# Performance work log

Hardware: AMD Instinct MI355X
Metric: run time of the kernel (lower is better)

The kernel has to match this reference:

```python
import jax, jax.numpy as jnp
import numpy as np

B, D, N, K, H = 8, 1024, 4096, 64, 512


def setup_inputs() -> dict:
    key = jax.random.key(0)
    ks = jax.random.split(key, 8)
    s1 = 1.0 / np.sqrt(D)
    s2 = 1.0 / np.sqrt(H)
    return {
        "feature": jax.random.normal(ks[0], (B, D, N), jnp.float32),
        "xyz": jax.random.normal(ks[1], (B, 3, N), jnp.float32),
        "w1": jax.random.normal(ks[2], (H, D), jnp.float32) * s1,
        "b1": jnp.zeros((H,), jnp.float32),
        "g1": jnp.ones((H,), jnp.float32),
        "be1": jnp.zeros((H,), jnp.float32),
        "w2": jax.random.normal(ks[3], (H, H), jnp.float32) * s2,
        "b2": jnp.zeros((H,), jnp.float32),
        "g2": jnp.ones((H,), jnp.float32),
        "be2": jnp.zeros((H,), jnp.float32),
        "w3": jax.random.normal(ks[4], (K, H), jnp.float32) * s2,
        "b3": jnp.zeros((K,), jnp.float32),
    }


def _conv1d(x, w, b):
    # pointwise Conv1d (kernel_size=1): [b,c,n] x [o,c] -> [b,o,n]
    return jnp.einsum('bcn,oc->bon', x, w) + b[None, :, None]


def _bn(x, g, be, eps=1e-5):
    # BatchNorm1d in training mode: batch statistics over (batch, spatial)
    m = x.mean(axis=(0, 2), keepdims=True)
    v = x.var(axis=(0, 2), keepdims=True)
    return (x - m) * jax.lax.rsqrt(v + eps) * g[None, :, None] + be[None, :, None]


def _regular(center, reg=1e-4):
    k = center.shape[-1]
    gram = jnp.einsum('bdm,bdn->bmn', center, center)
    return reg * jnp.abs(gram - jnp.eye(k, dtype=center.dtype)[None]).mean()


def _sinkhorn(cost, epsilon, max_iter):
    # log-domain Sinkhorn with uniform marginals; fixed iteration count
    b, n, m = cost.shape
    log_p = jnp.full((b, n), -np.log(n), cost.dtype)
    log_q = jnp.full((b, m), -np.log(m), cost.dtype)

    def M(u, v):
        return (-cost + u[:, :, None] + v[:, None, :]) / epsilon

    def body(i, uv):
        u, v = uv
        u = epsilon * (log_p - jax.nn.logsumexp(M(u, v), axis=-1)) + u
        v = epsilon * (log_q - jax.nn.logsumexp(M(u, v), axis=-2)) + v
        return (u, v)

    u0 = jnp.zeros((b, n), cost.dtype)
    v0 = jnp.zeros((b, m), cost.dtype)
    u, v = jax.lax.fori_loop(0, max_iter, body, (u0, v0))
    return jnp.exp(M(u, v))  # transport plan gamma [b,n,m]


def _ot_assign(x, y, epsilon=1e-3, max_iter=25, dst='fe'):
    # x: [b,d,n], y: [b,d,m]
    if dst == 'eu':
        xn = jnp.sum(x * x, axis=1)  # [b,n]
        yn = jnp.sum(y * y, axis=1)  # [b,m]
        cost = xn[:, :, None] + yn[:, None, :] - 2.0 * jnp.einsum('bdn,bdm->bnm', x, y)
    else:
        cost = 2.0 - 2.0 * jnp.einsum('bdn,bdm->bnm', x, y)
    return _sinkhorn(cost, epsilon, max_iter)


def _normalize(x, axis=1, eps=1e-12):
    nrm = jnp.linalg.norm(x, axis=axis, keepdims=True)
    return x / jnp.maximum(nrm, eps)


def reference(feature, xyz, w1, b1, g1, be1, w2, b2, g2, be2, w3, b3):
    b, d, n = feature.shape
    h = jax.nn.relu(_bn(_conv1d(feature, w1, b1), g1, be1))
    h = jax.nn.relu(_bn(_conv1d(h, w2, b2), g2, be2))
    log_score = _conv1d(h, w3, b3)  # [b,K,n]
    score = jax.nn.softmax(log_score, axis=1)
    pi = jax.lax.stop_gradient(jnp.maximum(score.sum(-1), 1e-4))[:, None, :]  # [b,1,K]

    # xyz branch
    mu_xyz = jnp.einsum('bkn,bdn->bdk', score, xyz) / pi  # [b,3,K]
    reg_xyz = 0.001 * _regular(mu_xyz)
    gamma_xyz = _ot_assign(jax.lax.stop_gradient(xyz), jax.lax.stop_gradient(mu_xyz), dst='eu')
    assign_xyz = jax.lax.stop_gradient(n * jnp.swapaxes(gamma_xyz, -1, -2))  # [b,K,n]

    # feature branch
    mu_fea = jnp.einsum('bkn,bdn->bdk', score, feature) / pi  # [b,D,K]
    n_feature = _normalize(feature)
    n_mu = _normalize(mu_fea)
    reg_fea = _regular(n_mu)
    gamma_fea = _ot_assign(jax.lax.stop_gradient(n_feature), jax.lax.stop_gradient(n_mu), dst='fe')
    assign_fea = jax.lax.stop_gradient(n * jnp.swapaxes(gamma_fea, -1, -2))  # [b,K,n]

    logp = jax.nn.log_softmax(log_score, axis=1)
    loss_xyz = -jnp.mean(jnp.sum(assign_xyz * logp, axis=1))
    loss_fea = -jnp.mean(jnp.sum(assign_fea * logp, axis=1))
    return loss_xyz + loss_fea + reg_fea + reg_xyz
```

## Files before the change

### kernel.cpp

```cpp
#include <hip/hip_runtime.h>
#include <math.h>

#define B_ 8
#define D_ 1024
#define N_ 4096
#define K_ 64
#define H_ 512

typedef short sx8 __attribute__((ext_vector_type(8)));
typedef float fx4 __attribute__((ext_vector_type(4)));

__device__ __forceinline__ float block_reduce_sum256(float v, float* sm) {
  int tid = threadIdx.x;
  sm[tid] = v;
  __syncthreads();
  for (int s = 128; s > 0; s >>= 1) {
    if (tid < s) sm[tid] += sm[tid + s];
    __syncthreads();
  }
  float r = sm[0];
  __syncthreads();
  return r;
}

__device__ __forceinline__ ushort f2bf(float f) {
  unsigned u = __float_as_uint(f);
  unsigned r = (u + 0x7fffu + ((u >> 16) & 1u)) >> 16;
  return (ushort)r;
}
__device__ __forceinline__ float bf2f(ushort h) {
  return __uint_as_float(((unsigned)h) << 16);
}

__global__ __launch_bounds__(256)
void split_w3(const float* __restrict__ W1, const float* __restrict__ W2,
              const float* __restrict__ W3, ushort* __restrict__ Wh1,
              ushort* __restrict__ Wl1, ushort* __restrict__ Wh2,
              ushort* __restrict__ Wl2, ushort* __restrict__ Wh3,
              ushort* __restrict__ Wl3) {
  int i = blockIdx.x * 256 + threadIdx.x;
  const float* W;
  ushort *Wh, *Wl;
  int o;
  if (i < 524288) { W = W1; Wh = Wh1; Wl = Wl1; o = i; }
  else if (i < 786432) { W = W2; Wh = Wh2; Wl = Wl2; o = i - 524288; }
  else { W = W3; Wh = Wh3; Wl = Wl3; o = i - 786432; }
  float f = W[o];
  ushort h = f2bf(f);
  Wh[o] = h;
  Wl[o] = f2bf(f - bf2f(h));
}

__global__ __launch_bounds__(256)
void transpose_split(const float* __restrict__ F, ushort* __restrict__ FhT,
                     ushort* __restrict__ FlT, float* __restrict__ nrmsq) {
  __shared__ float tile[64][65];
  __shared__ float nsq[64];
  int b = blockIdx.z, d0 = blockIdx.y * 64, n0 = blockIdx.x * 64;
  const float* src = F + ((long)b * D_ + d0) * N_ + n0;
  int t = threadIdx.x;
  if (t < 64) nsq[t] = 0.f;
  int rr4 = t >> 4, c4 = (t & 15) * 4;
#pragma unroll
  for (int p = 0; p < 4; ++p) {
    int dr = p * 16 + rr4;
    float4 v = *(const float4*)(src + (long)dr * N_ + c4);
    tile[dr][c4 + 0] = v.x;
    tile[dr][c4 + 1] = v.y;
    tile[dr][c4 + 2] = v.z;
    tile[dr][c4 + 3] = v.w;
  }
  __syncthreads();
  int nlb = t >> 3, ds = (t & 7) * 8;
#pragma unroll
  for (int p = 0; p < 2; ++p) {
    int nl = p * 32 + nlb;
    sx8 hv, lv;
    float sq = 0.f;
#pragma unroll
    for (int j = 0; j < 8; ++j) {
      float f = tile[ds + j][nl];
      sq += f * f;
      ushort h = f2bf(f);
      hv[j] = (short)h;
      lv[j] = (short)f2bf(f - bf2f(h));
    }
    atomicAdd(&nsq[nl], sq);
    long o = ((long)b * N_ + n0 + nl) * D_ + d0 + ds;
    *(sx8*)(FhT + o) = hv;
    *(sx8*)(FlT + o) = lv;
  }
  __syncthreads();
  if (t < 64) atomicAdd(&nrmsq[(long)b * N_ + n0 + t], nsq[t]);
}

__global__ __launch_bounds__(256)
void gemm_split_bf16(const ushort* __restrict__ Ah, const ushort* __restrict__ Al,
                     const ushort* __restrict__ BhT, const ushort* __restrict__ BlT,
                     float* __restrict__ C, const float* __restrict__ bias,
                     int N, int Kd, long sBT, long sC) {
  __shared__ ushort As[2][128][40];
  __shared__ ushort Bs[2][128][40];
  const int t = threadIdx.x;
  const int m0 = blockIdx.y * 128, n0 = blockIdx.x * 128;
  const long bo = (long)blockIdx.z * sBT;
  float* Cp = C + (long)blockIdx.z * sC;
  const int half = t >> 7, r = t & 127;
  const ushort* Asrc = (half ? Al : Ah) + (long)(m0 + r) * Kd;
  const ushort* Bsrc = (half ? BlT : BhT) + bo + (long)(n0 + r) * Kd;
  ushort* AsD = &As[half][r][0];
  ushort* BsD = &Bs[half][r][0];
  const int w = t >> 6, ln = t & 15, qd = (t & 63) >> 4;
  const int wm = w >> 1, wn = w & 1;

  fx4 acc[4][4];
#pragma unroll
  for (int i = 0; i < 4; ++i)
#pragma unroll
    for (int j = 0; j < 4; ++j) acc[i][j] = (fx4)0.f;

  for (int k0 = 0; k0 < Kd; k0 += 32) {
    uint4 a0 = *(const uint4*)(Asrc + k0);
    uint4 a1 = *(const uint4*)(Asrc + k0 + 8);
    uint4 a2 = *(const uint4*)(Asrc + k0 + 16);
    uint4 a3 = *(const uint4*)(Asrc + k0 + 24);
    uint4 b0 = *(const uint4*)(Bsrc + k0);
    uint4 b1 = *(const uint4*)(Bsrc + k0 + 8);
    uint4 b2 = *(const uint4*)(Bsrc + k0 + 16);
    uint4 b3 = *(const uint4*)(Bsrc + k0 + 24);
    __syncthreads();
    *(uint4*)(AsD + 0) = a0;
    *(uint4*)(AsD + 8) = a1;
    *(uint4*)(AsD + 16) = a2;
    *(uint4*)(AsD + 24) = a3;
    *(uint4*)(BsD + 0) = b0;
    *(uint4*)(BsD + 8) = b1;
    *(uint4*)(BsD + 16) = b2;
    *(uint4*)(BsD + 24) = b3;
    __syncthreads();
    sx8 ahf[4], alf[4], bhf[4], blf[4];
#pragma unroll
    for (int mt = 0; mt < 4; ++mt) {
      ahf[mt] = *(const sx8*)&As[0][wm * 64 + mt * 16 + ln][qd * 8];
      alf[mt] = *(const sx8*)&As[1][wm * 64 + mt * 16 + ln][qd * 8];
    }
#pragma unroll
    for (int nt = 0; nt < 4; ++nt) {
      bhf[nt] = *(const sx8*)&Bs[0][wn * 64 + nt * 16 + ln][qd * 8];
      blf[nt] = *(const sx8*)&Bs[1][wn * 64 + nt * 16 + ln][qd * 8];
    }
#pragma unroll
    for (int mt = 0; mt < 4; ++mt)
#pragma unroll
      for (int nt = 0; nt < 4; ++nt) {
        acc[mt][nt] = __builtin_amdgcn_mfma_f32_16x16x32_bf16(ahf[mt], bhf[nt], acc[mt][nt], 0, 0, 0);
        acc[mt][nt] = __builtin_amdgcn_mfma_f32_16x16x32_bf16(alf[mt], bhf[nt], acc[mt][nt], 0, 0, 0);
        acc[mt][nt] = __builtin_amdgcn_mfma_f32_16x16x32_bf16(ahf[mt], blf[nt], acc[mt][nt], 0, 0, 0);
      }
  }
#pragma unroll
  for (int mt = 0; mt < 4; ++mt) {
#pragma unroll
    for (int rr = 0; rr < 4; ++rr) {
      int row = m0 + wm * 64 + mt * 16 + qd * 4 + rr;
      float bb = bias[row];
#pragma unroll
      for (int nt = 0; nt < 4; ++nt) {
        int col = n0 + wn * 64 + nt * 16 + ln;
        Cp[(long)row * N + col] = acc[mt][nt][rr] + bb;
      }
    }
  }
}


__global__ __launch_bounds__(256)
void gemm64_bb(const ushort* __restrict__ Ah, const ushort* __restrict__ Al,
               const ushort* __restrict__ BhT, const ushort* __restrict__ BlT,
               float* __restrict__ C, const float* __restrict__ bias,
               int N, int Kd, long sBT, long sC) {
  __shared__ ushort As[2][64][40];
  __shared__ ushort Bs[2][128][40];
  const int t = threadIdx.x;
  const int n0 = blockIdx.x * 128;
  float* Cp = C + (long)blockIdx.z * sC;
  const int hB = t >> 7, rB = t & 127;
  const ushort* Bsrc = (hB ? BlT : BhT) + (long)blockIdx.z * sBT + (long)(n0 + rB) * Kd;
  ushort* BsD = &Bs[hB][rB][0];
  const bool doA = t < 128;
  const int hA = (t >> 6) & 1, rA = t & 63;
  const ushort* Asrc = (hA ? Al : Ah) + (long)rA * Kd;
  ushort* AsD = &As[hA][rA][0];
  const int w = t >> 6, ln = t & 15, qd = (t & 63) >> 4;
  const int wm = w >> 1, wn = w & 1;

  fx4 acc[2][4];
#pragma unroll
  for (int i = 0; i < 2; ++i)
#pragma unroll
    for (int j = 0; j < 4; ++j) acc[i][j] = (fx4)0.f;

  for (int k0 = 0; k0 < Kd; k0 += 32) {
    uint4 b0 = *(const uint4*)(Bsrc + k0);
    uint4 b1 = *(const uint4*)(Bsrc + k0 + 8);
    uint4 b2 = *(const uint4*)(Bsrc + k0 + 16);
    uint4 b3 = *(const uint4*)(Bsrc + k0 + 24);
    uint4 a0, a1, a2, a3;
    if (doA) {
      a0 = *(const uint4*)(Asrc + k0);
      a1 = *(const uint4*)(Asrc + k0 + 8);
      a2 = *(const uint4*)(Asrc + k0 + 16);
      a3 = *(const uint4*)(Asrc + k0 + 24);
    }
    __syncthreads();
    *(uint4*)(BsD + 0) = b0;
    *(uint4*)(BsD + 8) = b1;
    *(uint4*)(BsD + 16) = b2;
    *(uint4*)(BsD + 24) = b3;
    if (doA) {
      *(uint4*)(AsD + 0) = a0;
      *(uint4*)(AsD + 8) = a1;
      *(uint4*)(AsD + 16) = a2;
      *(uint4*)(AsD + 24) = a3;
    }
    __syncthreads();
    sx8 ahf[2], alf[2], bhf[4], blf[4];
#pragma unroll
    for (int mt = 0; mt < 2; ++mt) {
      ahf[mt] = *(const sx8*)&As[0][wm * 32 + mt * 16 + ln][qd * 8];
      alf[mt] = *(const sx8*)&As[1][wm * 32 + mt * 16 + ln][qd * 8];
    }
#pragma unroll
    for (int nt = 0; nt < 4; ++nt) {
      bhf[nt] = *(const sx8*)&Bs[0][wn * 64 + nt * 16 + ln][qd * 8];
      blf[nt] = *(const sx8*)&Bs[1][wn * 64 + nt * 16 + ln][qd * 8];
    }
#pragma unroll
    for (int mt = 0; mt < 2; ++mt)
#pragma unroll
      for (int nt = 0; nt < 4; ++nt) {
        acc[mt][nt] = __builtin_amdgcn_mfma_f32_16x16x32_bf16(ahf[mt], bhf[nt], acc[mt][nt], 0, 0, 0);
        acc[mt][nt] = __builtin_amdgcn_mfma_f32_16x16x32_bf16(alf[mt], bhf[nt], acc[mt][nt], 0, 0, 0);
        acc[mt][nt] = __builtin_amdgcn_mfma_f32_16x16x32_bf16(ahf[mt], blf[nt], acc[mt][nt], 0, 0, 0);
      }
  }
#pragma unroll
  for (int mt = 0; mt < 2; ++mt)
#pragma unroll
    for (int rr = 0; rr < 4; ++rr) {
      int row = wm * 32 + mt * 16 + qd * 4 + rr;
      float bb = bias[row];
#pragma unroll
      for (int nt = 0; nt < 4; ++nt) {
        int col = n0 + wn * 64 + nt * 16 + ln;
        Cp[(long)row * N + col] = acc[mt][nt][rr] + bb;
      }
    }
}

__global__ __launch_bounds__(256)
void gemm64_bf(const ushort* __restrict__ Ah, const ushort* __restrict__ Al,
               const float* __restrict__ Bf, float* __restrict__ Cacc) {
  __shared__ ushort As[2][64][40];
  __shared__ ushort Bs[2][128][40];
  const int t = threadIdx.x;
  const int nc0 = blockIdx.x * 128;
  const int kBeg = blockIdx.y * 1024;
  const int b = blockIdx.z;
  const int pc = t >> 7, rB = t & 127;
  const float* Bsrc = Bf + (long)b * D_ * N_ + (long)(nc0 + rB) * N_ + kBeg + pc * 16;
  const bool doA = t < 128;
  const int hA = (t >> 6) & 1, rA = t & 63;
  const ushort* Asrc = (hA ? Al : Ah) + (long)b * K_ * N_ + (long)rA * N_ + kBeg;
  ushort* AsD = &As[hA][rA][0];
  const int w = t >> 6, ln = t & 15, qd = (t & 63) >> 4;
  const int wm = w >> 1, wn = w & 1;

  fx4 acc[2][4];
#pragma unroll
  for (int i = 0; i < 2; ++i)
#pragma unroll
    for (int j = 0; j < 4; ++j) acc[i][j] = (fx4)0.f;

  for (int k0 = 0; k0 < 1024; k0 += 32) {
    float4 f0 = *(const float4*)(Bsrc + k0);
    float4 f1 = *(const float4*)(Bsrc + k0 + 4);
    float4 f2 = *(const float4*)(Bsrc + k0 + 8);
    float4 f3 = *(const float4*)(Bsrc + k0 + 12);
    uint4 a0, a1, a2, a3;
    if (doA) {
      a0 = *(const uint4*)(Asrc + k0);
      a1 = *(const uint4*)(Asrc + k0 + 8);
      a2 = *(const uint4*)(Asrc + k0 + 16);
      a3 = *(const uint4*)(Asrc + k0 + 24);
    }
    float fv[16] = {f0.x, f0.y, f0.z, f0.w, f1.x, f1.y, f1.z, f1.w,
                    f2.x, f2.y, f2.z, f2.w, f3.x, f3.y, f3.z, f3.w};
    sx8 hv0, hv1, lv0, lv1;
#pragma unroll
    for (int j = 0; j < 8; ++j) {
      ushort h = f2bf(fv[j]);
      hv0[j] = (short)h;
      lv0[j] = (short)f2bf(fv[j] - bf2f(h));
    }
#pragma unroll
    for (int j = 0; j < 8; ++j) {
      ushort h = f2bf(fv[8 + j]);
      hv1[j] = (short)h;
      lv1[j] = (short)f2bf(fv[8 + j] - bf2f(h));
    }
    __syncthreads();
    *(sx8*)&Bs[0][rB][pc * 16] = hv0;
    *(sx8*)&Bs[0][rB][pc * 16 + 8] = hv1;
    *(sx8*)&Bs[1][rB][pc * 16] = lv0;
    *(sx8*)&Bs[1][rB][pc * 16 + 8] = lv1;
    if (doA) {
      *(uint4*)(AsD + 0) = a0;
      *(uint4*)(AsD + 8) = a1;
      *(uint4*)(AsD + 16) = a2;
      *(uint4*)(AsD + 24) = a3;
    }
    __syncthreads();
    sx8 ahf[2], alf[2], bhf[4], blf[4];
#pragma unroll
    for (int mt = 0; mt < 2; ++mt) {
      ahf[mt] = *(const sx8*)&As[0][wm * 32 + mt * 16 + ln][qd * 8];
      alf[mt] = *(const sx8*)&As[1][wm * 32 + mt * 16 + ln][qd * 8];
    }
#pragma unroll
    for (int nt = 0; nt < 4; ++nt) {
      bhf[nt] = *(const sx8*)&Bs[0][wn * 64 + nt * 16 + ln][qd * 8];
      blf[nt] = *(const sx8*)&Bs[1][wn * 64 + nt * 16 + ln][qd * 8];
    }
#pragma unroll
    for (int mt = 0; mt < 2; ++mt)
#pragma unroll
      for (int nt = 0; nt < 4; ++nt) {
        acc[mt][nt] = __builtin_amdgcn_mfma_f32_16x16x32_bf16(ahf[mt], bhf[nt], acc[mt][nt], 0, 0, 0);
        acc[mt][nt] = __builtin_amdgcn_mfma_f32_16x16x32_bf16(alf[mt], bhf[nt], acc[mt][nt], 0, 0, 0);
        acc[mt][nt] = __builtin_amdgcn_mfma_f32_16x16x32_bf16(ahf[mt], blf[nt], acc[mt][nt], 0, 0, 0);
      }
  }
#pragma unroll
  for (int mt = 0; mt < 2; ++mt)
#pragma unroll
    for (int rr = 0; rr < 4; ++rr) {
      int row = wm * 32 + mt * 16 + qd * 4 + rr;
#pragma unroll
      for (int nt = 0; nt < 4; ++nt) {
        int col = nc0 + wn * 64 + nt * 16 + ln;
        atomicAdd(&Cacc[((long)b * K_ + row) * D_ + col], acc[mt][nt][rr]);
      }
    }
}

__global__ __launch_bounds__(256)
void gemm64_bt(const ushort* __restrict__ Ah, const ushort* __restrict__ Al,
               const float* __restrict__ Bf, const float* __restrict__ nrmsq,
               float* __restrict__ cost) {
  __shared__ ushort As[2][64][40];
  __shared__ ushort Bs[2][128][40];
  __shared__ float Ft[32][132];
  const int t = threadIdx.x;
  const int n0 = blockIdx.x * 128;
  const int b = blockIdx.z;
  const float* Fsrc = Bf + (long)b * D_ * N_;
  const bool doA = t < 128;
  const int hA = (t >> 6) & 1, rA = t & 63;
  const ushort* Asrc = (hA ? Al : Ah) + (long)b * K_ * D_ + (long)rA * D_;
  ushort* AsD = &As[hA][rA][0];
  const int dr = t >> 3, cc = (t & 7) * 16;
  const int nl = t & 127, dh = t >> 7;
  const int w = t >> 6, ln = t & 15, qd = (t & 63) >> 4;
  const int wm = w >> 1, wn = w & 1;

  fx4 acc[2][4];
#pragma unroll
  for (int i = 0; i < 2; ++i)
#pragma unroll
    for (int j = 0; j < 4; ++j) acc[i][j] = (fx4)0.f;

  for (int k0 = 0; k0 < D_; k0 += 32) {
    float4 f0 = *(const float4*)(Fsrc + (long)(k0 + dr) * N_ + n0 + cc);
    float4 f1 = *(const float4*)(Fsrc + (long)(k0 + dr) * N_ + n0 + cc + 4);
    float4 f2 = *(const float4*)(Fsrc + (long)(k0 + dr) * N_ + n0 + cc + 8);
    float4 f3 = *(const float4*)(Fsrc + (long)(k0 + dr) * N_ + n0 + cc + 12);
    uint4 a0, a1, a2, a3;
    if (doA) {
      a0 = *(const uint4*)(Asrc + k0);
      a1 = *(const uint4*)(Asrc + k0 + 8);
      a2 = *(const uint4*)(Asrc + k0 + 16);
      a3 = *(const uint4*)(Asrc + k0 + 24);
    }
    __syncthreads();
    *(float4*)&Ft[dr][cc] = f0;
    *(float4*)&Ft[dr][cc + 4] = f1;
    *(float4*)&Ft[dr][cc + 8] = f2;
    *(float4*)&Ft[dr][cc + 12] = f3;
    if (doA) {
      *(uint4*)(AsD + 0) = a0;
      *(uint4*)(AsD + 8) = a1;
      *(uint4*)(AsD + 16) = a2;
      *(uint4*)(AsD + 24) = a3;
    }
    __syncthreads();
    float fv[16];
#pragma unroll
    for (int j = 0; j < 16; ++j) fv[j] = Ft[dh * 16 + j][nl];
    sx8 hv0, hv1, lv0, lv1;
#pragma unroll
    for (int j = 0; j < 8; ++j) {
      ushort h = f2bf(fv[j]);
      hv0[j] = (short)h;
      lv0[j] = (short)f2bf(fv[j] - bf2f(h));
    }
#pragma unroll
    for (int j = 0; j < 8; ++j) {
      ushort h = f2bf(fv[8 + j]);
      hv1[j] = (short)h;
      lv1[j] = (short)f2bf(fv[8 + j] - bf2f(h));
    }
    *(sx8*)&Bs[0][nl][dh * 16] = hv0;
    *(sx8*)&Bs[0][nl][dh * 16 + 8] = hv1;
    *(sx8*)&Bs[1][nl][dh * 16] = lv0;
    *(sx8*)&Bs[1][nl][dh * 16 + 8] = lv1;
    __syncthreads();
    sx8 ahf[2], alf[2], bhf[4], blf[4];
#pragma unroll
    for (int mt = 0; mt < 2; ++mt) {
      ahf[mt] = *(const sx8*)&As[0][wm * 32 + mt * 16 + ln][qd * 8];
      alf[mt] = *(const sx8*)&As[1][wm * 32 + mt * 16 + ln][qd * 8];
    }
#pragma unroll
    for (int nt = 0; nt < 4; ++nt) {
      bhf[nt] = *(const sx8*)&Bs[0][wn * 64 + nt * 16 + ln][qd * 8];
      blf[nt] = *(const sx8*)&Bs[1][wn * 64 + nt * 16 + ln][qd * 8];
    }
#pragma unroll
    for (int mt = 0; mt < 2; ++mt)
#pragma unroll
      for (int nt = 0; nt < 4; ++nt) {
        acc[mt][nt] = __builtin_amdgcn_mfma_f32_16x16x32_bf16(ahf[mt], bhf[nt], acc[mt][nt], 0, 0, 0);
        acc[mt][nt] = __builtin_amdgcn_mfma_f32_16x16x32_bf16(alf[mt], bhf[nt], acc[mt][nt], 0, 0, 0);
        acc[mt][nt] = __builtin_amdgcn_mfma_f32_16x16x32_bf16(ahf[mt], blf[nt], acc[mt][nt], 0, 0, 0);
      }
  }
#pragma unroll
  for (int nt = 0; nt < 4; ++nt) {
    int col = n0 + wn * 64 + nt * 16 + ln;
    float q = nrmsq[b * N_ + col];
    float iv = 1.f / fmaxf(sqrtf(q), 1e-12f);
#pragma unroll
    for (int mt = 0; mt < 2; ++mt)
#pragma unroll
      for (int rr = 0; rr < 4; ++rr) {
        int row = wm * 32 + mt * 16 + qd * 4 + rr;
        cost[((long)b * K_ + row) * N_ + col] = 2.f - 2.f * acc[mt][nt][rr] * iv;
      }
  }
}

__global__ __launch_bounds__(256)
void bn_stats(const float* __restrict__ Y, const float* __restrict__ g,
              const float* __restrict__ be, float* __restrict__ scale,
              float* __restrict__ shift, int C) {
  int c = blockIdx.x;
  double s1 = 0.0, s2 = 0.0;
  for (int idx = threadIdx.x; idx < B_ * N_; idx += 256) {
    int b = idx >> 12, n = idx & (N_ - 1);
    float v = Y[((long)b * C + c) * N_ + n];
    s1 += v;
    s2 += (double)v * (double)v;
  }
  __shared__ double r1[256], r2[256];
  int tid = threadIdx.x;
  r1[tid] = s1; r2[tid] = s2;
  __syncthreads();
  for (int s = 128; s > 0; s >>= 1) {
    if (tid < s) { r1[tid] += r1[tid + s]; r2[tid] += r2[tid + s]; }
    __syncthreads();
  }
  if (tid == 0) {
    double m = r1[0] / (double)(B_ * N_);
    double var = r2[0] / (double)(B_ * N_) - m * m;
    float sc = (float)((double)g[c] / sqrt(var + 1e-5));
    scale[c] = sc;
    shift[c] = (float)((double)be[c] - m * (double)sc);
  }
}

__global__ __launch_bounds__(256)
void bn_relu_t(const float* __restrict__ Y, const float* __restrict__ scale,
               const float* __restrict__ shift, ushort* __restrict__ OhT,
               ushort* __restrict__ OlT) {
  __shared__ float tile[64][65];
  int b = blockIdx.z, h0 = blockIdx.y * 64, n0 = blockIdx.x * 64;
  const float* src = Y + ((long)b * H_ + h0) * N_ + n0;
  int t = threadIdx.x;
  int rr4 = t >> 4, c4 = (t & 15) * 4;
#pragma unroll
  for (int p = 0; p < 4; ++p) {
    int hl = p * 16 + rr4;
    float sc = scale[h0 + hl], sh = shift[h0 + hl];
    float4 v = *(const float4*)(src + (long)hl * N_ + c4);
    tile[hl][c4 + 0] = fmaxf(v.x * sc + sh, 0.f);
    tile[hl][c4 + 1] = fmaxf(v.y * sc + sh, 0.f);
    tile[hl][c4 + 2] = fmaxf(v.z * sc + sh, 0.f);
    tile[hl][c4 + 3] = fmaxf(v.w * sc + sh, 0.f);
  }
  __syncthreads();
  int nlb = t >> 3, hs = (t & 7) * 8;
#pragma unroll
  for (int p = 0; p < 2; ++p) {
    int nl = p * 32 + nlb;
    sx8 hv, lv;
#pragma unroll
    for (int j = 0; j < 8; ++j) {
      float f = tile[hs + j][nl];
      ushort h = f2bf(f);
      hv[j] = (short)h;
      lv[j] = (short)f2bf(f - bf2f(h));
    }
    long o = ((long)b * N_ + n0 + nl) * H_ + h0 + hs;
    *(sx8*)(OhT + o) = hv;
    *(sx8*)(OlT + o) = lv;
  }
}

__global__ __launch_bounds__(256)
void softmax_nk(const float* __restrict__ ls, float* __restrict__ scoreKN,
                ushort* __restrict__ sch, ushort* __restrict__ scl,
                float* __restrict__ logpNK, float* __restrict__ pi_raw) {
  __shared__ float L[64][65];
  __shared__ float ploc[64];
  int tid = threadIdx.x;
  if (tid < 64) ploc[tid] = 0.f;
  __syncthreads();
  int bi = blockIdx.x >> 4;
  int nb = (blockIdx.x & 15) * 256;
  int n = nb + tid;
  const float* x = ls + ((long)bi * K_) * N_ + n;
  float xv[64];
#pragma unroll
  for (int k = 0; k < 64; ++k) xv[k] = x[(long)k * N_];
  float mx = -1e30f;
#pragma unroll
  for (int k = 0; k < 64; ++k) mx = fmaxf(mx, xv[k]);
  float s = 0.f;
#pragma unroll
  for (int k = 0; k < 64; ++k) s += __expf(xv[k] - mx);
  float lg = __logf(s);
  float inv = 1.f / s;
#pragma unroll
  for (int k = 0; k < 64; ++k) {
    float sc = __expf(xv[k] - mx) * inv;
    long o = ((long)bi * K_ + k) * N_ + n;
    scoreKN[o] = sc;
    ushort h = f2bf(sc);
    sch[o] = h;
    scl[o] = f2bf(sc - bf2f(h));
    atomicAdd(&ploc[k], sc);
  }
  __syncthreads();
  if (tid < 64) atomicAdd(&pi_raw[bi * 64 + tid], ploc[tid]);
  int myw = tid >> 6, nl = tid & 63;
  int row = tid >> 2, ch = (tid & 3) * 16;
  for (int p = 0; p < 4; ++p) {
    __syncthreads();
    if (myw == p) {
#pragma unroll
      for (int k = 0; k < 64; ++k) L[nl][k] = xv[k] - mx - lg;
    }
    __syncthreads();
    float o0[16];
#pragma unroll
    for (int j = 0; j < 16; ++j) o0[j] = L[row][ch + j];
    float* dst = logpNK + ((long)bi * N_ + nb + p * 64 + row) * 64 + ch;
    *(float4*)(dst + 0) = make_float4(o0[0], o0[1], o0[2], o0[3]);
    *(float4*)(dst + 4) = make_float4(o0[4], o0[5], o0[6], o0[7]);
    *(float4*)(dst + 8) = make_float4(o0[8], o0[9], o0[10], o0[11]);
    *(float4*)(dst + 12) = make_float4(o0[12], o0[13], o0[14], o0[15]);
  }
}

__global__ __launch_bounds__(64)
void mu_xyz_k(const float* __restrict__ scoreKN, const float* __restrict__ xyz,
              const float* __restrict__ pi_raw, float* __restrict__ mu,
              float* __restrict__ yn) {
  int k = blockIdx.x, b = blockIdx.y, t = threadIdx.x;
  const float* st = scoreKN + ((long)b * K_ + k) * N_;
  const float* xp = xyz + (long)b * 3 * N_;
  float a0 = 0, a1 = 0, a2 = 0;
  for (int n = t; n < N_; n += 64) {
    float s = st[n];
    a0 += s * xp[n];
    a1 += s * xp[N_ + n];
    a2 += s * xp[2 * N_ + n];
  }
  for (int off = 32; off > 0; off >>= 1) {
    a0 += __shfl_down(a0, off);
    a1 += __shfl_down(a1, off);
    a2 += __shfl_down(a2, off);
  }
  if (t == 0) {
    float p = fmaxf(pi_raw[b * K_ + k], 1e-4f);
    float m0 = a0 / p, m1 = a1 / p, m2 = a2 / p;
    mu[((long)b * 3 + 0) * K_ + k] = m0;
    mu[((long)b * 3 + 1) * K_ + k] = m1;
    mu[((long)b * 3 + 2) * K_ + k] = m2;
    yn[b * K_ + k] = m0 * m0 + m1 * m1 + m2 * m2;
  }
}

__global__ __launch_bounds__(256)
void reg_xyz_k(const float* __restrict__ mu, float* __restrict__ out) {
  __shared__ float red[256];
  int b = blockIdx.x, tid = threadIdx.x;
  float acc = 0.f;
  for (int e = tid; e < 4096; e += 256) {
    int m = e >> 6, n2 = e & 63;
    float g = 0.f;
    for (int d = 0; d < 3; ++d)
      g += mu[((long)b * 3 + d) * K_ + m] * mu[((long)b * 3 + d) * K_ + n2];
    acc += fabsf(g - (m == n2 ? 1.f : 0.f));
  }
  float tot = block_reduce_sum256(acc, red);
  if (tid == 0) atomicAdd(out, tot * (1e-7f / 32768.f));
}

__global__ __launch_bounds__(256)
void reg_fea_k(const float* __restrict__ nT, float* __restrict__ out) {
  __shared__ float pm[1024];
  __shared__ float red[256];
  int m = blockIdx.x, b = blockIdx.y, tid = threadIdx.x;
  const float* base = nT + (long)b * K_ * D_;
  *(float4*)&pm[tid * 4] = *(const float4*)(base + (long)m * D_ + tid * 4);
  __syncthreads();
  int n2 = tid >> 2, q = tid & 3;
  const float* pn = base + (long)n2 * D_ + q * 256;
  const float* pml = &pm[q * 256];
  float g = 0.f;
#pragma unroll 8
  for (int d = 0; d < 256; d += 4) {
    float4 v = *(const float4*)(pn + d);
    g += v.x * pml[d] + v.y * pml[d + 1] + v.z * pml[d + 2] + v.w * pml[d + 3];
  }
  g += __shfl_down(g, 2);
  g += __shfl_down(g, 1);
  float acc = (q == 0) ? fabsf(g - (m == n2 ? 1.f : 0.f)) : 0.f;
  float tot = block_reduce_sum256(acc, red);
  if (tid == 0) atomicAdd(out, tot * (1e-4f / 32768.f));
}

__global__ __launch_bounds__(256)
void mu_finalize(const float* __restrict__ muT_raw, const float* __restrict__ pi_raw,
                 float* __restrict__ n_muT, ushort* __restrict__ nmu_h,
                 ushort* __restrict__ nmu_l) {
  __shared__ float red[256];
  int k = blockIdx.x, b = blockIdx.y, tid = threadIdx.x;
  float p = fmaxf(pi_raw[b * K_ + k], 1e-4f);
  const float* src = muT_raw + ((long)b * K_ + k) * D_;
  float ss = 0.f;
  for (int d = tid; d < D_; d += 256) {
    float v = src[d] / p;
    ss += v * v;
  }
  float tot = block_reduce_sum256(ss, red);
  float inv = 1.f / fmaxf(sqrtf(tot), 1e-12f);
  long o = ((long)b * K_ + k) * D_;
  for (int d = tid; d < D_; d += 256) {
    float v = src[d] / p * inv;
    n_muT[o + d] = v;
    ushort h = f2bf(v);
    nmu_h[o + d] = h;
    nmu_l[o + d] = f2bf(v - bf2f(h));
  }
}

__global__ __launch_bounds__(256, 1)
void sinkhorn_coop(const float* __restrict__ cost_f, const float* __restrict__ xyz,
                   const float* __restrict__ mu, const float* __restrict__ yn,
                   const float* __restrict__ logpNK, float* __restrict__ out,
                   unsigned long long* __restrict__ partMS,
                   unsigned int* __restrict__ seq) {
  __shared__ float tile[4][64][68];
  __shared__ float vsh[64];
  __shared__ float wm[4][64];
  __shared__ float wsum[4][64];
  __shared__ float red[256];
  __shared__ float mub[4][64];
  const int tid = threadIdx.x;
  const int g = blockIdx.x & 15;
  const int s = blockIdx.x >> 4;
  const int w = tid >> 6, lane = tid & 63;
  const int i = s * 256 + tid;
  const int b = g & 7;
  const float eps = 1e-3f, ti = 1000.0f;
  const float lgp = -8.317766166719343f;
  const float lgq = -4.1588830833596715f;

  float c[64];
  if (g < 8) {
    if (tid < 64) {
      mub[0][tid] = mu[(b * 3 + 0) * K_ + tid];
      mub[1][tid] = mu[(b * 3 + 1) * K_ + tid];
      mub[2][tid] = mu[(b * 3 + 2) * K_ + tid];
      mub[3][tid] = yn[b * K_ + tid];
      vsh[tid] = 0.f;
    }
    __syncthreads();
    float x0 = xyz[((long)b * 3 + 0) * N_ + i];
    float x1 = xyz[((long)b * 3 + 1) * N_ + i];
    float x2 = xyz[((long)b * 3 + 2) * N_ + i];
    float xn = x0 * x0 + x1 * x1 + x2 * x2;
#pragma unroll
    for (int j = 0; j < 64; ++j)
      c[j] = xn + mub[3][j] - 2.f * (x0 * mub[0][j] + x1 * mub[1][j] + x2 * mub[2][j]);
  } else {
    const float* C = cost_f + (long)b * K_ * N_;
#pragma unroll
    for (int j = 0; j < 64; ++j) c[j] = C[(long)j * N_ + i];
    if (tid < 64) vsh[tid] = 0.f;
    __syncthreads();
  }
  float u = 0.f;

  for (int it = 0; it < 25; ++it) {
    float tj[64];
#pragma unroll
    for (int j = 0; j < 64; ++j) tj[j] = vsh[j] - c[j];
    float dm = -1e30f;
#pragma unroll
    for (int j = 0; j < 64; ++j) dm = fmaxf(dm, tj[j]);
    float ssum = 0.f;
#pragma unroll
    for (int j = 0; j < 64; ++j) ssum += __expf((tj[j] - dm) * ti);
    u = eps * (lgp - ((u + dm) * ti + __logf(ssum))) + u;
#pragma unroll
    for (int j4 = 0; j4 < 16; ++j4) {
      float4 v4;
      v4.x = (u + tj[j4 * 4 + 0]) * ti;
      v4.y = (u + tj[j4 * 4 + 1]) * ti;
      v4.z = (u + tj[j4 * 4 + 2]) * ti;
      v4.w = (u + tj[j4 * 4 + 3]) * ti;
      *(float4*)&tile[w][lane][j4 * 4] = v4;
    }
    __syncthreads();
    float M = -1e30f, S = 0.f;
#pragma unroll
    for (int r = 0; r < 64; ++r) {
      float a = tile[w][r][lane];
      M = fmaxf(M, a);
      S += __expf(a - lgp);
    }
    wm[w][lane] = M;
    wsum[w][lane] = S;
    __syncthreads();
    int buf = it & 1;
    if (tid < 64) {
      float Mb = fmaxf(fmaxf(wm[0][tid], wm[1][tid]), fmaxf(wm[2][tid], wm[3][tid]));
      float Sb = wsum[0][tid] + wsum[1][tid] + wsum[2][tid] + wsum[3][tid];
      unsigned long long pk =
          ((unsigned long long)__float_as_uint(Sb) << 32) | (unsigned long long)__float_as_uint(Mb);
      long idx = (((long)buf * 16 + g) * 16 + s) * 64 + tid;
      __hip_atomic_store(&partMS[idx], pk, __ATOMIC_RELAXED, __HIP_MEMORY_SCOPE_AGENT);
    }
    __syncthreads();
    unsigned target = (unsigned)(it + 1);
    if (tid == 0)
      __hip_atomic_store(&seq[((long)g * 16 + s) * 32], target, __ATOMIC_RELEASE,
                         __HIP_MEMORY_SCOPE_AGENT);
    if (tid < 16) {
      while (__hip_atomic_load(&seq[((long)g * 16 + tid) * 32], __ATOMIC_ACQUIRE,
                               __HIP_MEMORY_SCOPE_AGENT) < target)
        __builtin_amdgcn_s_sleep(1);
    }
    __syncthreads();
    if (tid < 64) {
      long base = (((long)buf * 16 + g) * 16) * 64 + tid;
      float M2 = -1e30f, S2 = 0.f;
#pragma unroll
      for (int p = 0; p < 16; ++p) {
        unsigned long long v =
            __hip_atomic_load(&partMS[base + (long)p * 64], __ATOMIC_RELAXED, __HIP_MEMORY_SCOPE_AGENT);
        M2 = fmaxf(M2, __uint_as_float((unsigned)v));
        S2 += __uint_as_float((unsigned)(v >> 32));
      }
      float lsec = fmaxf(M2, lgp + __logf(S2));
      vsh[tid] = eps * (lgq - lsec) + vsh[tid];
    }
    __syncthreads();
  }

  const float* lp = logpNK + ((long)b * N_ + i) * 64;
  float part = 0.f;
#pragma unroll
  for (int j = 0; j < 64; ++j)
    part += __expf((u + vsh[j] - c[j]) * ti) * lp[j];
  red[tid] = part;
  __syncthreads();
  for (int st2 = 128; st2 > 0; st2 >>= 1) {
    if (tid < st2) red[tid] += red[tid + st2];
    __syncthreads();
  }
  if (tid == 0) atomicAdd(out, -red[0] / (float)B_);
}

extern "C" void kernel_launch(void* const* d_in, const int* in_sizes, int n_in,
                              void* d_out, int out_size, void* d_ws, size_t ws_size,
                              hipStream_t stream) {
  const float* feature = (const float*)d_in[0];
  const float* xyz = (const float*)d_in[1];
  const float* w1 = (const float*)d_in[2];
  const float* b1 = (const float*)d_in[3];
  const float* g1 = (const float*)d_in[4];
  const float* be1 = (const float*)d_in[5];
  const float* w2 = (const float*)d_in[6];
  const float* b2 = (const float*)d_in[7];
  const float* g2 = (const float*)d_in[8];
  const float* be2 = (const float*)d_in[9];
  const float* w3 = (const float*)d_in[10];
  const float* b3 = (const float*)d_in[11];
  float* out = (float*)d_out;
  float* ws = (float*)d_ws;

  const long RSZ = 16777216L;
  float* regA = ws;
  float* regB1 = ws + RSZ;
  float* regB2 = ws + 2 * RSZ;
  float* sm = ws + 3 * RSZ;

  ushort* FhT = (ushort*)regB1;
  ushort* FlT = (ushort*)regB2;
  float* h1raw = regA;
  ushort* h1hT = (ushort*)regB1;
  ushort* h1lT = (ushort*)regB1 + RSZ;
  float* h2 = regB2;
  ushort* h2hT = (ushort*)regB1;
  ushort* h2lT = (ushort*)regB1 + RSZ;
  const long sz = (long)B_ * N_ * K_;
  float* log_score = regA;
  float* score_KN = regA + sz;
  float* logpNK = regA + 2 * sz;
  float* cost_f = regA + 3 * sz;
  ushort* sc_h = (ushort*)(regA + 4 * sz);
  ushort* sc_l = (ushort*)(regA + 4 * sz) + sz;

  ushort* Wh1 = (ushort*)sm; sm += 262144;
  ushort* Wl1 = (ushort*)sm; sm += 262144;
  ushort* Wh2 = (ushort*)sm; sm += 131072;
  ushort* Wl2 = (ushort*)sm; sm += 131072;
  ushort* Wh3 = (ushort*)sm; sm += 16384;
  ushort* Wl3 = (ushort*)sm; sm += 16384;
  float* muT_raw = sm; sm += (long)B_ * K_ * D_;
  float* n_muT = sm;   sm += (long)B_ * K_ * D_;
  ushort* nmu_h = (ushort*)sm; sm += 262144;
  ushort* nmu_l = (ushort*)sm; sm += 262144;
  unsigned long long* partMS = (unsigned long long*)sm; sm += 2 * 16 * 16 * 64 * 2;
  unsigned int* seq = (unsigned int*)sm; sm += 16 * 16 * 32;
  float* nrmsq = sm; sm += (long)B_ * N_;
  float* mu_x = sm;   sm += 2048;
  float* yn = sm;     sm += 512;
  float* pi_raw = sm; sm += 512;
  float* sc1 = sm; sm += 512;
  float* sh1 = sm; sm += 512;
  float* sc2 = sm; sm += 512;
  float* sh2 = sm; sm += 512;

  hipMemsetAsync(d_out, 0, sizeof(float) * out_size, stream);
  hipMemsetAsync(pi_raw, 0, 512 * sizeof(float), stream);
  hipMemsetAsync(seq, 0, 16 * 16 * 32 * sizeof(unsigned int), stream);
  hipMemsetAsync(muT_raw, 0, (long)B_ * K_ * D_ * sizeof(float), stream);
  hipMemsetAsync(nrmsq, 0, (long)B_ * N_ * sizeof(float), stream);

  split_w3<<<3200, 256, 0, stream>>>(w1, w2, w3, Wh1, Wl1, Wh2, Wl2, Wh3, Wl3);
  {
    dim3 g(N_ / 64, D_ / 64, B_);
    transpose_split<<<g, 256, 0, stream>>>(feature, FhT, FlT, nrmsq);
  }
  {
    dim3 g(N_ / 128, H_ / 128, B_);
    gemm_split_bf16<<<g, 256, 0, stream>>>(Wh1, Wl1, FhT, FlT, h1raw, b1,
                                           N_, D_, (long)N_ * D_, (long)H_ * N_);
  }
  bn_stats<<<H_, 256, 0, stream>>>(h1raw, g1, be1, sc1, sh1, H_);
  {
    dim3 g(N_ / 64, H_ / 64, B_);
    bn_relu_t<<<g, 256, 0, stream>>>(h1raw, sc1, sh1, h1hT, h1lT);
  }
  {
    dim3 g(N_ / 128, H_ / 128, B_);
    gemm_split_bf16<<<g, 256, 0, stream>>>(Wh2, Wl2, h1hT, h1lT, h2, b2,
                                           N_, H_, (long)N_ * H_, (long)H_ * N_);
  }
  bn_stats<<<H_, 256, 0, stream>>>(h2, g2, be2, sc2, sh2, H_);
  {
    dim3 g(N_ / 64, H_ / 64, B_);
    bn_relu_t<<<g, 256, 0, stream>>>(h2, sc2, sh2, h2hT, h2lT);
  }
  {
    dim3 g(N_ / 128, 1, B_);
    gemm64_bb<<<g, 256, 0, stream>>>(Wh3, Wl3, h2hT, h2lT, log_score, b3,
                                     N_, H_, (long)N_ * H_, (long)K_ * N_);
  }
  softmax_nk<<<B_ * N_ / 256, 256, 0, stream>>>(log_score, score_KN, sc_h, sc_l,
                                                logpNK, pi_raw);
  {
    dim3 g(K_, B_);
    mu_xyz_k<<<g, 64, 0, stream>>>(score_KN, xyz, pi_raw, mu_x, yn);
  }
  reg_xyz_k<<<B_, 256, 0, stream>>>(mu_x, out);
  {
    dim3 g(D_ / 128, 4, B_);
    gemm64_bf<<<g, 256, 0, stream>>>(sc_h, sc_l, feature, muT_raw);
  }
  {
    dim3 g(K_, B_);
    mu_finalize<<<g, 256, 0, stream>>>(muT_raw, pi_raw, n_muT, nmu_h, nmu_l);
  }
  {
    dim3 g(K_, B_);
    reg_fea_k<<<g, 256, 0, stream>>>(n_muT, out);
  }
  {
    dim3 g(N_ / 128, 1, B_);
    gemm64_bt<<<g, 256, 0, stream>>>(nmu_h, nmu_l, feature, nrmsq, cost_f);
  }
  {
    void* kargs[] = {(void*)&cost_f, (void*)&xyz, (void*)&mu_x, (void*)&yn,
                     (void*)&logpNK, (void*)&out, (void*)&partMS, (void*)&seq};
    hipLaunchCooperativeKernel((const void*)sinkhorn_coop, dim3(256), dim3(256),
                               kargs, 0, stream);
  }
}
```

Baseline: 1.189 ms.

## Fuse transpose/bf16 split and BN-ReLU into GEMM loaders, BN stats into epilogue

The GEMMs now read fp32 activations straight from global memory, apply BN scale/shift and ReLU, split values into bf16 hi/lo, and write them transposed into shared memory. This removes the separate transpose_split and bn_relu_t passes. BatchNorm sums and sums of squares are accumulated in the GEMM epilogue with shuffles and atomics, and a tiny bn_fin kernel replaces the per-channel bn_stats kernel. In exchange, each GEMM block redoes the conversion work for every M tile, and variance is now computed in fp32 from atomically summed moments instead of in double, which lowers numerical precision.

```diff
diff --git a/kernel.cpp b/kernel.cpp
--- a/kernel.cpp
+++ b/kernel.cpp
@@ -52,66 +52,32 @@
 }
 
 __global__ __launch_bounds__(256)
-void transpose_split(const float* __restrict__ F, ushort* __restrict__ FhT,
-                     ushort* __restrict__ FlT, float* __restrict__ nrmsq) {
-  __shared__ float tile[64][65];
-  __shared__ float nsq[64];
-  int b = blockIdx.z, d0 = blockIdx.y * 64, n0 = blockIdx.x * 64;
-  const float* src = F + ((long)b * D_ + d0) * N_ + n0;
-  int t = threadIdx.x;
-  if (t < 64) nsq[t] = 0.f;
-  int rr4 = t >> 4, c4 = (t & 15) * 4;
-#pragma unroll
-  for (int p = 0; p < 4; ++p) {
-    int dr = p * 16 + rr4;
-    float4 v = *(const float4*)(src + (long)dr * N_ + c4);
-    tile[dr][c4 + 0] = v.x;
-    tile[dr][c4 + 1] = v.y;
-    tile[dr][c4 + 2] = v.z;
-    tile[dr][c4 + 3] = v.w;
-  }
-  __syncthreads();
-  int nlb = t >> 3, ds = (t & 7) * 8;
-#pragma unroll
-  for (int p = 0; p < 2; ++p) {
-    int nl = p * 32 + nlb;
-    sx8 hv, lv;
-    float sq = 0.f;
-#pragma unroll
-    for (int j = 0; j < 8; ++j) {
-      float f = tile[ds + j][nl];
-      sq += f * f;
-      ushort h = f2bf(f);
-      hv[j] = (short)h;
-      lv[j] = (short)f2bf(f - bf2f(h));
-    }
-    atomicAdd(&nsq[nl], sq);
-    long o = ((long)b * N_ + n0 + nl) * D_ + d0 + ds;
-    *(sx8*)(FhT + o) = hv;
-    *(sx8*)(FlT + o) = lv;
-  }
-  __syncthreads();
-  if (t < 64) atomicAdd(&nrmsq[(long)b * N_ + n0 + t], nsq[t]);
-}
-
-__global__ __launch_bounds__(256)
-void gemm_split_bf16(const ushort* __restrict__ Ah, const ushort* __restrict__ Al,
-                     const ushort* __restrict__ BhT, const ushort* __restrict__ BlT,
-                     float* __restrict__ C, const float* __restrict__ bias,
-                     int N, int Kd, long sBT, long sC) {
+void conv_bt128(const ushort* __restrict__ Ah, const ushort* __restrict__ Al,
+                const float* __restrict__ Bf, const float* __restrict__ scale,
+                const float* __restrict__ shift, float* __restrict__ C,
+                const float* __restrict__ bias, float* __restrict__ rs,
+                float* __restrict__ rss, float* __restrict__ nrm,
+                int Kd, long sB, long sC) {
   __shared__ ushort As[2][128][40];
   __shared__ ushort Bs[2][128][40];
+  __shared__ float Ft[32][132];
+  __shared__ float scb[32], shb[32];
+  __shared__ float rs_l[128], rss_l[128];
   const int t = threadIdx.x;
-  const int m0 = blockIdx.y * 128, n0 = blockIdx.x * 128;
-  const long bo = (long)blockIdx.z * sBT;
-  float* Cp = C + (long)blockIdx.z * sC;
-  const int half = t >> 7, r = t & 127;
-  const ushort* Asrc = (half ? Al : Ah) + (long)(m0 + r) * Kd;
-  const ushort* Bsrc = (half ? BlT : BhT) + bo + (long)(n0 + r) * Kd;
-  ushort* AsD = &As[half][r][0];
-  ushort* BsD = &Bs[half][r][0];
+  const int n0 = blockIdx.x * 128;
+  const int m0 = blockIdx.y * 128;
+  const int b = blockIdx.z;
+  const float* Fsrc = Bf + (long)b * sB;
+  float* Cp = C + (long)b * sC;
+  const int half = t >> 7, rA = t & 127;
+  const ushort* Asrc = (half ? Al : Ah) + (long)(m0 + rA) * Kd;
+  ushort* AsD = &As[half][rA][0];
+  const int dr = t >> 3, cc = (t & 7) * 16;
+  const int nl = t & 127, dh = t >> 7;
   const int w = t >> 6, ln = t & 15, qd = (t & 63) >> 4;
   const int wm = w >> 1, wn = w & 1;
+  if (t < 128) { rs_l[t] = 0.f; rss_l[t] = 0.f; }
+  float nsq = 0.f;
 
   fx4 acc[4][4];
 #pragma unroll
@@ -120,23 +86,53 @@
     for (int j = 0; j < 4; ++j) acc[i][j] = (fx4)0.f;
 
   for (int k0 = 0; k0 < Kd; k0 += 32) {
+    float4 f0 = *(const float4*)(Fsrc + (long)(k0 + dr) * N_ + n0 + cc);
+    float4 f1 = *(const float4*)(Fsrc + (long)(k0 + dr) * N_ + n0 + cc + 4);
+    float4 f2 = *(const float4*)(Fsrc + (long)(k0 + dr) * N_ + n0 + cc + 8);
+    float4 f3 = *(const float4*)(Fsrc + (long)(k0 + dr) * N_ + n0 + cc + 12);
     uint4 a0 = *(const uint4*)(Asrc + k0);
     uint4 a1 = *(const uint4*)(Asrc + k0 + 8);
     uint4 a2 = *(const uint4*)(Asrc + k0 + 16);
     uint4 a3 = *(const uint4*)(Asrc + k0 + 24);
-    uint4 b0 = *(const uint4*)(Bsrc + k0);
-    uint4 b1 = *(const uint4*)(Bsrc + k0 + 8);
-    uint4 b2 = *(const uint4*)(Bsrc + k0 + 16);
-    uint4 b3 = *(const uint4*)(Bsrc + k0 + 24);
-    __syncthreads();
+    __syncthreads();
+    *(float4*)&Ft[dr][cc] = f0;
+    *(float4*)&Ft[dr][cc + 4] = f1;
+    *(float4*)&Ft[dr][cc + 8] = f2;
+    *(float4*)&Ft[dr][cc + 12] = f3;
     *(uint4*)(AsD + 0) = a0;
     *(uint4*)(AsD + 8) = a1;
     *(uint4*)(AsD + 16) = a2;
     *(uint4*)(AsD + 24) = a3;
-    *(uint4*)(BsD + 0) = b0;
-    *(uint4*)(BsD + 8) = b1;
-    *(uint4*)(BsD + 16) = b2;
-    *(uint4*)(BsD + 24) = b3;
+    if (t < 32) {
+      scb[t] = scale ? scale[k0 + t] : 1.f;
+      shb[t] = scale ? shift[k0 + t] : 0.f;
+    }
+    __syncthreads();
+    float fv[16];
+#pragma unroll
+    for (int j = 0; j < 16; ++j) {
+      float v = Ft[dh * 16 + j][nl];
+      if (scale) v = fmaxf(v * scb[dh * 16 + j] + shb[dh * 16 + j], 0.f);
+      fv[j] = v;
+      nsq += v * v;
+    }
+    sx8 hv0, hv1, lv0, lv1;
+#pragma unroll
+    for (int j = 0; j < 8; ++j) {
+      ushort h = f2bf(fv[j]);
+      hv0[j] = (short)h;
+      lv0[j] = (short)f2bf(fv[j] - bf2f(h));
+    }
+#pragma unroll
+    for (int j = 0; j < 8; ++j) {
+      ushort h = f2bf(fv[8 + j]);
+      hv1[j] = (short)h;
+      lv1[j] = (short)f2bf(fv[8 + j] - bf2f(h));
+    }
+    *(sx8*)&Bs[0][nl][dh * 16] = hv0;
+    *(sx8*)&Bs[0][nl][dh * 16 + 8] = hv1;
+    *(sx8*)&Bs[1][nl][dh * 16] = lv0;
+    *(sx8*)&Bs[1][nl][dh * 16 + 8] = lv1;
     __syncthreads();
     sx8 ahf[4], alf[4], bhf[4], blf[4];
 #pragma unroll
@@ -162,35 +158,76 @@
   for (int mt = 0; mt < 4; ++mt) {
 #pragma unroll
     for (int rr = 0; rr < 4; ++rr) {
-      int row = m0 + wm * 64 + mt * 16 + qd * 4 + rr;
+      int rloc = wm * 64 + mt * 16 + qd * 4 + rr;
+      int row = m0 + rloc;
       float bb = bias[row];
+      float s1 = 0.f, s2 = 0.f;
 #pragma unroll
       for (int nt = 0; nt < 4; ++nt) {
         int col = n0 + wn * 64 + nt * 16 + ln;
-        Cp[(long)row * N + col] = acc[mt][nt][rr] + bb;
+        float y = acc[mt][nt][rr] + bb;
+        Cp[(long)row * N_ + col] = y;
+        s1 += y;
+        s2 += y * y;
       }
-    }
-  }
-}
-
+      if (rs) {
+#pragma unroll
+        for (int m = 1; m < 16; m <<= 1) {
+          s1 += __shfl_xor(s1, m);
+          s2 += __shfl_xor(s2, m);
+        }
+        if (ln == 0) {
+          atomicAdd(&rs_l[rloc], s1);
+          atomicAdd(&rss_l[rloc], s2);
+        }
+      }
+    }
+  }
+  if (nrm && blockIdx.y == 0)
+    atomicAdd(&nrm[(long)b * N_ + n0 + nl], nsq);
+  if (rs) {
+    __syncthreads();
+    if (t < 128) {
+      atomicAdd(&rs[m0 + t], rs_l[t]);
+      atomicAdd(&rss[m0 + t], rss_l[t]);
+    }
+  }
+}
+
+__global__ void bn_fin(const float* __restrict__ rs, const float* __restrict__ rss,
+                       const float* __restrict__ g, const float* __restrict__ be,
+                       float* __restrict__ sc, float* __restrict__ sh) {
+  int c = blockIdx.x * 256 + threadIdx.x;
+  if (c < H_) {
+    float inv = 1.f / (float)(B_ * N_);
+    float m = rs[c] * inv;
+    float var = rss[c] * inv - m * m;
+    float s = g[c] * rsqrtf(var + 1e-5f);
+    sc[c] = s;
+    sh[c] = be[c] - m * s;
+  }
+}
 
 __global__ __launch_bounds__(256)
-void gemm64_bb(const ushort* __restrict__ Ah, const ushort* __restrict__ Al,
-               const ushort* __restrict__ BhT, const ushort* __restrict__ BlT,
-               float* __restrict__ C, const float* __restrict__ bias,
-               int N, int Kd, long sBT, long sC) {
+void conv64_bn(const ushort* __restrict__ Ah, const ushort* __restrict__ Al,
+               const float* __restrict__ Bf, const float* __restrict__ scale,
+               const float* __restrict__ shift, float* __restrict__ C,
+               const float* __restrict__ bias, int Kd, long sB, long sC) {
   __shared__ ushort As[2][64][40];
   __shared__ ushort Bs[2][128][40];
+  __shared__ float Ft[32][132];
+  __shared__ float scb[32], shb[32];
   const int t = threadIdx.x;
   const int n0 = blockIdx.x * 128;
-  float* Cp = C + (long)blockIdx.z * sC;
-  const int hB = t >> 7, rB = t & 127;
-  const ushort* Bsrc = (hB ? BlT : BhT) + (long)blockIdx.z * sBT + (long)(n0 + rB) * Kd;
-  ushort* BsD = &Bs[hB][rB][0];
+  const int b = blockIdx.z;
+  const float* Fsrc = Bf + (long)b * sB;
+  float* Cp = C + (long)b * sC;
   const bool doA = t < 128;
   const int hA = (t >> 6) & 1, rA = t & 63;
   const ushort* Asrc = (hA ? Al : Ah) + (long)rA * Kd;
   ushort* AsD = &As[hA][rA][0];
+  const int dr = t >> 3, cc = (t & 7) * 16;
+  const int nl = t & 127, dh = t >> 7;
   const int w = t >> 6, ln = t & 15, qd = (t & 63) >> 4;
   const int wm = w >> 1, wn = w & 1;
 
@@ -201,10 +238,10 @@
     for (int j = 0; j < 4; ++j) acc[i][j] = (fx4)0.f;
 
   for (int k0 = 0; k0 < Kd; k0 += 32) {
-    uint4 b0 = *(const uint4*)(Bsrc + k0);
-    uint4 b1 = *(const uint4*)(Bsrc + k0 + 8);
-    uint4 b2 = *(const uint4*)(Bsrc + k0 + 16);
-    uint4 b3 = *(const uint4*)(Bsrc + k0 + 24);
+    float4 f0 = *(const float4*)(Fsrc + (long)(k0 + dr) * N_ + n0 + cc);
+    float4 f1 = *(const float4*)(Fsrc + (long)(k0 + dr) * N_ + n0 + cc + 4);
+    float4 f2 = *(const float4*)(Fsrc + (long)(k0 + dr) * N_ + n0 + cc + 8);
+    float4 f3 = *(const float4*)(Fsrc + (long)(k0 + dr) * N_ + n0 + cc + 12);
     uint4 a0, a1, a2, a3;
     if (doA) {
       a0 = *(const uint4*)(Asrc + k0);
@@ -213,16 +250,44 @@
       a3 = *(const uint4*)(Asrc + k0 + 24);
     }
     __syncthreads();
-    *(uint4*)(BsD + 0) = b0;
-    *(uint4*)(BsD + 8) = b1;
-    *(uint4*)(BsD + 16) = b2;
-    *(uint4*)(BsD + 24) = b3;
+    *(float4*)&Ft[dr][cc] = f0;
+    *(float4*)&Ft[dr][cc + 4] = f1;
+    *(float4*)&Ft[dr][cc + 8] = f2;
+    *(float4*)&Ft[dr][cc + 12] = f3;
     if (doA) {
       *(uint4*)(AsD + 0) = a0;
       *(uint4*)(AsD + 8) = a1;
       *(uint4*)(AsD + 16) = a2;
       *(uint4*)(AsD + 24) = a3;
     }
+    if (t < 32) {
+      scb[t] = scale[k0 + t];
+      shb[t] = shift[k0 + t];
+    }
+    __syncthreads();
+    float fv[16];
+#pragma unroll
+    for (int j = 0; j < 16; ++j) {
+      float v = Ft[dh * 16 + j][nl];
+      fv[j] = fmaxf(v * scb[dh * 16 + j] + shb[dh * 16 + j], 0.f);
+    }
+    sx8 hv0, hv1, lv0, lv1;
+#pragma unroll
+    for (int j = 0; j < 8; ++j) {
+      ushort h = f2bf(fv[j]);
+      hv0[j] = (short)h;
+      lv0[j] = (short)f2bf(fv[j] - bf2f(h));
+    }
+#pragma unroll
+    for (int j = 0; j < 8; ++j) {
+      ushort h = f2bf(fv[8 + j]);
+      hv1[j] = (short)h;
+      lv1[j] = (short)f2bf(fv[8 + j] - bf2f(h));
+    }
+    *(sx8*)&Bs[0][nl][dh * 16] = hv0;
+    *(sx8*)&Bs[0][nl][dh * 16 + 8] = hv1;
+    *(sx8*)&Bs[1][nl][dh * 16] = lv0;
+    *(sx8*)&Bs[1][nl][dh * 16 + 8] = lv1;
     __syncthreads();
     sx8 ahf[2], alf[2], bhf[4], blf[4];
 #pragma unroll
@@ -253,7 +318,7 @@
 #pragma unroll
       for (int nt = 0; nt < 4; ++nt) {
         int col = n0 + wn * 64 + nt * 16 + ln;
-        Cp[(long)row * N + col] = acc[mt][nt][rr] + bb;
+        Cp[(long)row * N_ + col] = acc[mt][nt][rr] + bb;
       }
     }
 }
@@ -457,73 +522,6 @@
         int row = wm * 32 + mt * 16 + qd * 4 + rr;
         cost[((long)b * K_ + row) * N_ + col] = 2.f - 2.f * acc[mt][nt][rr] * iv;
       }
-  }
-}
-
-__global__ __launch_bounds__(256)
-void bn_stats(const float* __restrict__ Y, const float* __restrict__ g,
-              const float* __restrict__ be, float* __restrict__ scale,
-              float* __restrict__ shift, int C) {
-  int c = blockIdx.x;
-  double s1 = 0.0, s2 = 0.0;
-  for (int idx = threadIdx.x; idx < B_ * N_; idx += 256) {
-    int b = idx >> 12, n = idx & (N_ - 1);
-    float v = Y[((long)b * C + c) * N_ + n];
-    s1 += v;
-    s2 += (double)v * (double)v;
-  }
-  __shared__ double r1[256], r2[256];
-  int tid = threadIdx.x;
-  r1[tid] = s1; r2[tid] = s2;
-  __syncthreads();
-  for (int s = 128; s > 0; s >>= 1) {
-    if (tid < s) { r1[tid] += r1[tid + s]; r2[tid] += r2[tid + s]; }
-    __syncthreads();
-  }
-  if (tid == 0) {
-    double m = r1[0] / (double)(B_ * N_);
-    double var = r2[0] / (double)(B_ * N_) - m * m;
-    float sc = (float)((double)g[c] / sqrt(var + 1e-5));
-    scale[c] = sc;
-    shift[c] = (float)((double)be[c] - m * (double)sc);
-  }
-}
-
-__global__ __launch_bounds__(256)
-void bn_relu_t(const float* __restrict__ Y, const float* __restrict__ scale,
-               const float* __restrict__ shift, ushort* __restrict__ OhT,
-               ushort* __restrict__ OlT) {
-  __shared__ float tile[64][65];
-  int b = blockIdx.z, h0 = blockIdx.y * 64, n0 = blockIdx.x * 64;
-  const float* src = Y + ((long)b * H_ + h0) * N_ + n0;
-  int t = threadIdx.x;
-  int rr4 = t >> 4, c4 = (t & 15) * 4;
-#pragma unroll
-  for (int p = 0; p < 4; ++p) {
-    int hl = p * 16 + rr4;
-    float sc = scale[h0 + hl], sh = shift[h0 + hl];
-    float4 v = *(const float4*)(src + (long)hl * N_ + c4);
-    tile[hl][c4 + 0] = fmaxf(v.x * sc + sh, 0.f);
-    tile[hl][c4 + 1] = fmaxf(v.y * sc + sh, 0.f);
-    tile[hl][c4 + 2] = fmaxf(v.z * sc + sh, 0.f);
-    tile[hl][c4 + 3] = fmaxf(v.w * sc + sh, 0.f);
-  }
-  __syncthreads();
-  int nlb = t >> 3, hs = (t & 7) * 8;
-#pragma unroll
-  for (int p = 0; p < 2; ++p) {
-    int nl = p * 32 + nlb;
-    sx8 hv, lv;
-#pragma unroll
-    for (int j = 0; j < 8; ++j) {
-      float f = tile[hs + j][nl];
-      ushort h = f2bf(f);
-      hv[j] = (short)h;
-      lv[j] = (short)f2bf(f - bf2f(h));
-    }
-    long o = ((long)b * N_ + n0 + nl) * H_ + h0 + hs;
-    *(sx8*)(OhT + o) = hv;
-    *(sx8*)(OlT + o) = lv;
   }
 }
 
@@ -827,17 +825,10 @@
   const long RSZ = 16777216L;
   float* regA = ws;
   float* regB1 = ws + RSZ;
-  float* regB2 = ws + 2 * RSZ;
   float* sm = ws + 3 * RSZ;
 
-  ushort* FhT = (ushort*)regB1;
-  ushort* FlT = (ushort*)regB2;
   float* h1raw = regA;
-  ushort* h1hT = (ushort*)regB1;
-  ushort* h1lT = (ushort*)regB1 + RSZ;
-  float* h2 = regB2;
-  ushort* h2hT = (ushort*)regB1;
-  ushort* h2lT = (ushort*)regB1 + RSZ;
+  float* h2raw = regB1;
   const long sz = (long)B_ * N_ * K_;
   float* log_score = regA;
   float* score_KN = regA + sz;
@@ -862,6 +853,10 @@
   float* mu_x = sm;   sm += 2048;
   float* yn = sm;     sm += 512;
   float* pi_raw = sm; sm += 512;
+  float* rs1 = sm; sm += 512;
+  float* rss1 = sm; sm += 512;
+  float* rs2 = sm; sm += 512;
+  float* rss2 = sm; sm += 512;
   float* sc1 = sm; sm += 512;
   float* sh1 = sm; sm += 512;
   float* sc2 = sm; sm += 512;
@@ -872,36 +867,27 @@
   hipMemsetAsync(seq, 0, 16 * 16 * 32 * sizeof(unsigned int), stream);
   hipMemsetAsync(muT_raw, 0, (long)B_ * K_ * D_ * sizeof(float), stream);
   hipMemsetAsync(nrmsq, 0, (long)B_ * N_ * sizeof(float), stream);
+  hipMemsetAsync(rs1, 0, 4 * 512 * sizeof(float), stream);
 
   split_w3<<<3200, 256, 0, stream>>>(w1, w2, w3, Wh1, Wl1, Wh2, Wl2, Wh3, Wl3);
   {
-    dim3 g(N_ / 64, D_ / 64, B_);
-    transpose_split<<<g, 256, 0, stream>>>(feature, FhT, FlT, nrmsq);
-  }
+    dim3 g(N_ / 128, H_ / 128, B_);
+    conv_bt128<<<g, 256, 0, stream>>>(Wh1, Wl1, feature, nullptr, nullptr, h1raw,
+                                      b1, rs1, rss1, nrmsq, D_, (long)D_ * N_,
+                                      (long)H_ * N_);
+  }
+  bn_fin<<<2, 256, 0, stream>>>(rs1, rss1, g1, be1, sc1, sh1);
   {
     dim3 g(N_ / 128, H_ / 128, B_);
-    gemm_split_bf16<<<g, 256, 0, stream>>>(Wh1, Wl1, FhT, FlT, h1raw, b1,
-                                           N_, D_, (long)N_ * D_, (long)H_ * N_);
-  }
-  bn_stats<<<H_, 256, 0, stream>>>(h1raw, g1, be1, sc1, sh1, H_);
-  {
-    dim3 g(N_ / 64, H_ / 64, B_);
-    bn_relu_t<<<g, 256, 0, stream>>>(h1raw, sc1, sh1, h1hT, h1lT);
-  }
-  {
-    dim3 g(N_ / 128, H_ / 128, B_);
-    gemm_split_bf16<<<g, 256, 0, stream>>>(Wh2, Wl2, h1hT, h1lT, h2, b2,
-                                           N_, H_, (long)N_ * H_, (long)H_ * N_);
-  }
-  bn_stats<<<H_, 256, 0, stream>>>(h2, g2, be2, sc2, sh2, H_);
-  {
-    dim3 g(N_ / 64, H_ / 64, B_);
-    bn_relu_t<<<g, 256, 0, stream>>>(h2, sc2, sh2, h2hT, h2lT);
-  }
+    conv_bt128<<<g, 256, 0, stream>>>(Wh2, Wl2, h1raw, sc1, sh1, h2raw, b2, rs2,
+                                      rss2, nullptr, H_, (long)H_ * N_,
+                                      (long)H_ * N_);
+  }
+  bn_fin<<<2, 256, 0, stream>>>(rs2, rss2, g2, be2, sc2, sh2);
   {
     dim3 g(N_ / 128, 1, B_);
-    gemm64_bb<<<g, 256, 0, stream>>>(Wh3, Wl3, h2hT, h2lT, log_score, b3,
-                                     N_, H_, (long)N_ * H_, (long)K_ * N_);
+    conv64_bn<<<g, 256, 0, stream>>>(Wh3, Wl3, h2raw, sc2, sh2, log_score, b3,
+                                     H_, (long)H_ * N_, (long)K_ * N_);
   }
   softmax_nk<<<B_ * N_ / 256, 256, 0, stream>>>(log_score, score_KN, sc_h, sc_l,
                                                 logpNK, pi_raw);
```

Result: faster. 1.076 ms (-9.5%).
